# Kernel optimization log

Hardware: AMD Instinct MI355X
Metric: run time of the kernel (lower is better)

## Reference

```python
import jax, jax.numpy as jnp
from jax import lax
import numpy as np


def setup_inputs() -> dict:
    key = jax.random.key(0)
    k1, k2, k3, k4 = jax.random.split(key, 4)
    x = jax.random.normal(k1, (16, 128, 128, 128), dtype=jnp.float32)
    weight = jax.random.normal(k2, (128, 128, 3, 3), dtype=jnp.float32)      # ITPLConv.weight (d, c, kh, kw)
    depth_w = jax.random.normal(k3, (128,), dtype=jnp.float32)               # depthwise 1x1 conv weight (c,1,1,1) flattened
    point_w = jax.random.normal(k4, (128, 128), dtype=jnp.float32)           # pointwise 1x1 conv weight (out, in)
    return {"x": x, "weight": weight, "depth_w": depth_w, "point_w": point_w}


def reference(x, weight, depth_w, point_w):
    # ZeroPad2d(padding=1) on H and W
    xp = jnp.pad(x, ((0, 0), (0, 0), (1, 1), (1, 1)))
    # substract2: unfold(x) - x[:,:,:uh,:uw] broadcast, contracted with weight.
    # Algebraically: conv2d(xp, W, stride=1, VALID) - einsum(xp_crop, W.sum(kh,kw))
    conv = lax.conv_general_dilated(
        xp, weight, window_strides=(1, 1), padding="VALID",
        dimension_numbers=("NCHW", "OIHW", "NCHW"))
    uh, uw = conv.shape[2], conv.shape[3]
    wsum = jnp.sum(weight, axis=(2, 3))                      # (d, c)
    corr = jnp.einsum("nchw,dc->ndhw", xp[:, :, :uh, :uw], wsum)
    sub = conv - corr                                        # (n, d, uh, uw)
    # DWconv: depthwise 1x1 (per-channel scale) then pointwise 1x1
    y = sub * depth_w[None, :, None, None]
    out = jnp.einsum("nchw,oc->nohw", y, point_w)
    return out
```

## Files before the change

kernel.cpp:

```cpp
#include <hip/hip_runtime.h>
#include <hip/hip_bf16.h>


typedef __attribute__((ext_vector_type(8))) short bf16x8;
typedef __attribute__((ext_vector_type(4))) float f32x4;

__device__ inline unsigned short f2bf(float f) {
    unsigned u = __builtin_bit_cast(unsigned, f);
    return (unsigned short)((u + 0x7FFFu + ((u >> 16) & 1u)) >> 16);
}

__device__ inline void gll16(const void* g, void* l) {
    __builtin_amdgcn_global_load_lds((const __attribute__((address_space(1))) void*)g,
                                     (__attribute__((address_space(3))) void*)l, 16, 0, 0);
}

__global__ void fuse_weights_bf16(const float* __restrict__ W,
                                  const float* __restrict__ dw,
                                  const float* __restrict__ P,
                                  unsigned short* __restrict__ w2b) {
    const int c = blockIdx.x;
    const int o = threadIdx.x;
    float acc[9];
#pragma unroll
    for (int t = 0; t < 9; ++t) acc[t] = 0.f;
    for (int d = 0; d < 128; ++d) {
        const float s = P[o * 128 + d] * dw[d];
        const float* wp = W + (size_t)(d * 128 + c) * 9;
        float tsum = 0.f;
#pragma unroll
        for (int t = 0; t < 9; ++t) {
            const float wv = wp[t];
            acc[t] = fmaf(s, wv, acc[t]);
            tsum += wv;
        }
        acc[0] = fmaf(-s, tsum, acc[0]);
    }
#pragma unroll
    for (int t = 0; t < 9; ++t)
        w2b[(t * 128 + o) * 128 + c] = f2bf(acc[t]);
}

__global__ __launch_bounds__(256) void to_nhwc_bf16(const float* __restrict__ x,
                                                    unsigned short* __restrict__ xb,
                                                    unsigned short* __restrict__ zrow) {
    __shared__ __attribute__((aligned(16))) unsigned short ys[128 * 130];
    const int h = blockIdx.x, n = blockIdx.y, tid = (int)threadIdx.x;

    for (int u = tid; u < 4096; u += 256) {
        const int c = u >> 5, w4 = (u & 31) * 4;
        float4 v = *reinterpret_cast<const float4*>(
            x + ((((size_t)n * 128 + c) * 128 + h) * 128 + w4));
        unsigned p0 = (unsigned)f2bf(v.x) | ((unsigned)f2bf(v.y) << 16);
        unsigned p1 = (unsigned)f2bf(v.z) | ((unsigned)f2bf(v.w) << 16);
        *reinterpret_cast<unsigned*>(&ys[c * 130 + w4]) = p0;
        *reinterpret_cast<unsigned*>(&ys[c * 130 + w4 + 2]) = p1;
    }
    __syncthreads();
    for (int u = tid; u < 2048; u += 256) {
        const int w = u >> 4, c8 = u & 15;
        bf16x8 st;
#pragma unroll
        for (int j = 0; j < 8; ++j) st[j] = (short)ys[(c8 * 8 + j) * 130 + w];
        *reinterpret_cast<bf16x8*>(
            xb + ((((size_t)n * 128 + h) * 128 + w) * 128 + c8 * 8)) = st;
    }
    if (h == 0 && n == 0) {
        bf16x8 z = 0;
        for (int u = tid; u < 2048; u += 256)
            *reinterpret_cast<bf16x8*>(zrow + u * 8) = z;
    }
}

#define LDS_CHUNK (3 * 132 * 32)

__global__ __launch_bounds__(256) void itpl_mfma_kernel(
    const unsigned short* __restrict__ xb,
    const unsigned short* __restrict__ w2b,
    const unsigned short* __restrict__ zrow,
    float* __restrict__ out) {
    __shared__ __attribute__((aligned(16))) unsigned short lds[2][LDS_CHUNK];

    const int bid = (int)blockIdx.x;
    const int lin = (bid & 7) * 256 + (bid >> 3);
    const int h = lin & 127, n = lin >> 7;

    const int tid = (int)threadIdx.x;
    const int l = tid & 63, wid = tid >> 6;
    const int wr = wid >> 1, wc = wid & 1;

    f32x4 acc[4][4];
#pragma unroll
    for (int i = 0; i < 4; ++i)
#pragma unroll
        for (int j = 0; j < 4; ++j) acc[i][j] = {0.f, 0.f, 0.f, 0.f};

    if (tid < 48) {
        const int slot = tid & 3, row = tid >> 2;
        const int buf = row / 6, rr = row % 6, r = rr >> 1, wi = (rr & 1) ? 129 : 0;
        bf16x8 z = 0;
        *reinterpret_cast<bf16x8*>(&lds[buf][(r * 132 + wi) * 32 + slot * 8]) = z;
    }

    const size_t nbase = (size_t)n * 128;

    auto stage = [&](int buf, int c0) {
        for (int s = wid * 6; s < wid * 6 + 6; ++s) {
            const int r = s >> 3, seg = s & 7;
            const int hr = h + r - 1;
            const int wl = seg * 16 + (l >> 2);
            const int wi = 1 + wl;
            const int q = (l & 3) ^ ((wi >> 1) & 3);
            const unsigned short* src;
            if ((unsigned)hr < 128u)
                src = xb + (((nbase + hr) * 128 + wl) * 128) + c0 + q * 8;
            else
                src = zrow + (wl * 128 + c0 + q * 8);
            gll16(src, (void*)&lds[buf][(r * 132 + 1 + seg * 16) * 32]);
        }
    };

    auto compute = [&](int buf, int c0) {
        const unsigned short* lb = &lds[buf][0];
#pragma unroll
        for (int t = 0; t < 9; ++t) {
            const int r = t / 3, kw = t % 3;
            bf16x8 bfr[4], afr[4];
#pragma unroll
            for (int ni = 0; ni < 4; ++ni) {
                const int o = wc * 64 + ni * 16 + (l & 15);
                bfr[ni] = *reinterpret_cast<const bf16x8*>(
                    w2b + ((t * 128 + o) * 128 + c0 + (l >> 4) * 8));
            }
#pragma unroll
            for (int mi = 0; mi < 4; ++mi) {
                const int wi = 1 + wr * 64 + mi * 16 + (l & 15) + kw - 1;
                const int slot = (l >> 4) ^ ((wi >> 1) & 3);
                afr[mi] = *reinterpret_cast<const bf16x8*>(
                    lb + (r * 132 + wi) * 32 + slot * 8);
            }
#pragma unroll
            for (int mi = 0; mi < 4; ++mi)
#pragma unroll
                for (int ni = 0; ni < 4; ++ni)
                    acc[mi][ni] = __builtin_amdgcn_mfma_f32_16x16x32_bf16(
                        afr[mi], bfr[ni], acc[mi][ni], 0, 0, 0);
        }
    };

    stage(0, 0);
    __syncthreads();
#pragma unroll
    for (int k = 0; k < 4; ++k) {
        if (k < 3) stage((k + 1) & 1, (k + 1) * 32);
        compute(k & 1, k * 32);
        __syncthreads();
    }

    const size_t ob = (nbase * 128 + h) * 128;
#pragma unroll
    for (int mi = 0; mi < 4; ++mi) {
        const int w = wr * 64 + mi * 16 + (l >> 4) * 4;
#pragma unroll
        for (int ni = 0; ni < 4; ++ni) {
            const int o = wc * 64 + ni * 16 + (l & 15);
            *reinterpret_cast<f32x4*>(out + ob + (size_t)o * 128 * 128 + w) = acc[mi][ni];
        }
    }
}

#define CB 32
__global__ void fuse_weights_kernel(const float* __restrict__ W,
                                    const float* __restrict__ dw,
                                    const float* __restrict__ P,
                                    float* __restrict__ W2) {
    const int c = blockIdx.x;
    const int o = threadIdx.x;
    float acc[9];
#pragma unroll
    for (int t = 0; t < 9; ++t) acc[t] = 0.f;
    for (int d = 0; d < 128; ++d) {
        const float s = P[o * 128 + d] * dw[d];
        const float* wp = W + (size_t)(d * 128 + c) * 9;
        float tsum = 0.f;
#pragma unroll
        for (int t = 0; t < 9; ++t) {
            const float wv = wp[t];
            acc[t] = fmaf(s, wv, acc[t]);
            tsum += wv;
        }
        acc[0] = fmaf(-s, tsum, acc[0]);
    }
#pragma unroll
    for (int t = 0; t < 9; ++t) W2[(c * 9 + t) * 128 + o] = acc[t];
}

__global__ __launch_bounds__(256) void itpl_conv_kernel(const float* __restrict__ x,
                                                        const float* __restrict__ W2,
                                                        float* __restrict__ out) {
    __shared__ float xs[CB][3][132];
    const int h = blockIdx.x;
    const int n = blockIdx.y;
    const int tid = (int)threadIdx.x;
    const int pg = tid & 15;
    const int og = tid >> 4;
    float acc[8][8];
#pragma unroll
    for (int i = 0; i < 8; ++i)
#pragma unroll
        for (int p = 0; p < 8; ++p) acc[i][p] = 0.f;
    for (int c0 = 0; c0 < 128; c0 += CB) {
        __syncthreads();
        for (int g = tid; g < CB * 3 * 32; g += 256) {
            const int f4 = g & 31;
            const int row = g >> 5;
            const int r = row % 3;
            const int c = row / 3;
            const int hr = h + r - 1;
            float4 v = make_float4(0.f, 0.f, 0.f, 0.f);
            if ((unsigned)hr < 128u)
                v = *reinterpret_cast<const float4*>(
                    x + ((((size_t)n * 128 + c0 + c) * 128 + hr) * 128 + f4 * 4));
            float* dst = &xs[c][r][1 + f4 * 4];
            dst[0] = v.x; dst[1] = v.y; dst[2] = v.z; dst[3] = v.w;
        }
        if (tid < CB * 3) {
            const int r = tid % 3;
            const int c = tid / 3;
            xs[c][r][0] = 0.f;
            xs[c][r][129] = 0.f;
        }
        __syncthreads();
        for (int c = 0; c < CB; ++c) {
#pragma unroll
            for (int kh = 0; kh < 3; ++kh) {
                float xr[12];
                const float* xsp = &xs[c][kh][pg * 8];
                *reinterpret_cast<float4*>(&xr[0]) = *reinterpret_cast<const float4*>(xsp);
                *reinterpret_cast<float4*>(&xr[4]) = *reinterpret_cast<const float4*>(xsp + 4);
                *reinterpret_cast<float4*>(&xr[8]) = *reinterpret_cast<const float4*>(xsp + 8);
#pragma unroll
                for (int kw = 0; kw < 3; ++kw) {
                    const float* wp = W2 + (size_t)((c0 + c) * 9 + kh * 3 + kw) * 128 + og * 8;
                    float wv[8];
                    *reinterpret_cast<float4*>(&wv[0]) = *reinterpret_cast<const float4*>(wp);
                    *reinterpret_cast<float4*>(&wv[4]) = *reinterpret_cast<const float4*>(wp + 4);
#pragma unroll
                    for (int i = 0; i < 8; ++i)
#pragma unroll
                        for (int p = 0; p < 8; ++p)
                            acc[i][p] = fmaf(wv[i], xr[p + kw], acc[i][p]);
                }
            }
        }
    }
#pragma unroll
    for (int i = 0; i < 8; ++i) {
        float* op = out + ((((size_t)n * 128 + og * 8 + i) * 128 + h) * 128 + pg * 8);
        *reinterpret_cast<float4*>(op)     = make_float4(acc[i][0], acc[i][1], acc[i][2], acc[i][3]);
        *reinterpret_cast<float4*>(op + 4) = make_float4(acc[i][4], acc[i][5], acc[i][6], acc[i][7]);
    }
}

extern "C" void kernel_launch(void* const* d_in, const int* in_sizes, int n_in,
                              void* d_out, int out_size, void* d_ws, size_t ws_size,
                              hipStream_t stream) {
    const float* x  = (const float*)d_in[0];
    const float* W  = (const float*)d_in[1];
    const float* dw = (const float*)d_in[2];
    const float* P  = (const float*)d_in[3];
    float* out = (float*)d_out;

    const size_t XB_BYTES = 67108864ull;
    const size_t ZR_BYTES = 32768ull;
    const size_t W2B_BYTES = 294912ull;
    if (ws_size >= XB_BYTES + ZR_BYTES + W2B_BYTES) {
        unsigned short* xbw  = (unsigned short*)d_ws;
        unsigned short* zrow = (unsigned short*)((char*)d_ws + XB_BYTES);
        unsigned short* w2b  = (unsigned short*)((char*)d_ws + XB_BYTES + ZR_BYTES);
        fuse_weights_bf16<<<128, 128, 0, stream>>>(W, dw, P, w2b);
        to_nhwc_bf16<<<dim3(128, 16), 256, 0, stream>>>(x, xbw, zrow);
        itpl_mfma_kernel<<<2048, 256, 0, stream>>>(xbw, w2b, zrow, out);
    } else {
        float* W2 = (float*)d_ws;
        fuse_weights_kernel<<<128, 128, 0, stream>>>(W, dw, P, W2);
        itpl_conv_kernel<<<dim3(128, 16), 256, 0, stream>>>(x, W2, out);
    }
}
```

Baseline: 420.9 us.

## Rework NHWC transpose LDS layout, batch weight loads, add occupancy hint

The NCHW-to-NHWC bf16 conversion now packs channel pairs into 32-bit words. It transposes through a padded LDS tile, so the write-out can use single 16-byte LDS reads instead of eight scalar gathers. The main MFMA kernel gets a launch_bounds occupancy hint of 2 blocks per SM. Its inner loop now fetches weight fragments for all three kw taps of a kernel row up front, to expose more memory-level parallelism. The bigger register footprint from the prefetched weights may conflict with the occupancy hint and cause spills.

```diff
diff --git a/kernel.cpp b/kernel.cpp
--- a/kernel.cpp
+++ b/kernel.cpp
@@ -4,6 +4,7 @@
 
 typedef __attribute__((ext_vector_type(8))) short bf16x8;
 typedef __attribute__((ext_vector_type(4))) float f32x4;
+typedef __attribute__((ext_vector_type(2))) unsigned int u32x2;
 
 __device__ inline unsigned short f2bf(float f) {
     unsigned u = __builtin_bit_cast(unsigned, f);
@@ -44,27 +45,44 @@
 __global__ __launch_bounds__(256) void to_nhwc_bf16(const float* __restrict__ x,
                                                     unsigned short* __restrict__ xb,
                                                     unsigned short* __restrict__ zrow) {
-    __shared__ __attribute__((aligned(16))) unsigned short ys[128 * 130];
+    __shared__ __attribute__((aligned(16))) unsigned ys[128 * 68];
     const int h = blockIdx.x, n = blockIdx.y, tid = (int)threadIdx.x;
-
-    for (int u = tid; u < 4096; u += 256) {
-        const int c = u >> 5, w4 = (u & 31) * 4;
-        float4 v = *reinterpret_cast<const float4*>(
-            x + ((((size_t)n * 128 + c) * 128 + h) * 128 + w4));
-        unsigned p0 = (unsigned)f2bf(v.x) | ((unsigned)f2bf(v.y) << 16);
-        unsigned p1 = (unsigned)f2bf(v.z) | ((unsigned)f2bf(v.w) << 16);
-        *reinterpret_cast<unsigned*>(&ys[c * 130 + w4]) = p0;
-        *reinterpret_cast<unsigned*>(&ys[c * 130 + w4 + 2]) = p1;
+    const int wv = tid >> 6, l = tid & 63;
+
+#pragma unroll
+    for (int i = 0; i < 4; ++i) {
+        const int wh = (i & 1) * 64;
+        const int CB0 = (2 * wv + (i >> 1)) * 16;
+        const int c0 = CB0 + 4 * (l >> 4);
+        const int w0 = wh + 4 * (l & 15);
+
+        float4 v[4];
+#pragma unroll
+        for (int r = 0; r < 4; ++r)
+            v[r] = *reinterpret_cast<const float4*>(
+                x + ((((size_t)n * 128 + c0 + r) * 128 + h) * 128 + w0));
+
+        const float* vf = reinterpret_cast<const float*>(v);
+#pragma unroll
+        for (int j = 0; j < 4; ++j) {
+            unsigned u0 = (unsigned)f2bf(vf[0 * 4 + j]) | ((unsigned)f2bf(vf[1 * 4 + j]) << 16);
+            unsigned u1 = (unsigned)f2bf(vf[2 * 4 + j]) | ((unsigned)f2bf(vf[3 * 4 + j]) << 16);
+            u32x2 st; st[0] = u0; st[1] = u1;
+            *reinterpret_cast<u32x2*>(&ys[(w0 + j) * 68 + (c0 >> 1)]) = st;
+        }
     }
     __syncthreads();
-    for (int u = tid; u < 2048; u += 256) {
-        const int w = u >> 4, c8 = u & 15;
-        bf16x8 st;
-#pragma unroll
-        for (int j = 0; j < 8; ++j) st[j] = (short)ys[(c8 * 8 + j) * 130 + w];
+
+#pragma unroll
+    for (int k = 0; k < 8; ++k) {
+        const int u = tid + 256 * k;
+        const int c8 = u & 15, w = u >> 4;
+        bf16x8 val = *reinterpret_cast<const bf16x8*>(
+            reinterpret_cast<const unsigned short*>(ys) + w * 136 + c8 * 8);
         *reinterpret_cast<bf16x8*>(
-            xb + ((((size_t)n * 128 + h) * 128 + w) * 128 + c8 * 8)) = st;
-    }
+            xb + ((((size_t)n * 128 + h) * 128 + w) * 128 + c8 * 8)) = val;
+    }
+
     if (h == 0 && n == 0) {
         bf16x8 z = 0;
         for (int u = tid; u < 2048; u += 256)
@@ -74,7 +92,7 @@
 
 #define LDS_CHUNK (3 * 132 * 32)
 
-__global__ __launch_bounds__(256) void itpl_mfma_kernel(
+__global__ __launch_bounds__(256, 2) void itpl_mfma_kernel(
     const unsigned short* __restrict__ xb,
     const unsigned short* __restrict__ w2b,
     const unsigned short* __restrict__ zrow,
@@ -123,28 +141,34 @@
     auto compute = [&](int buf, int c0) {
         const unsigned short* lb = &lds[buf][0];
 #pragma unroll
-        for (int t = 0; t < 9; ++t) {
-            const int r = t / 3, kw = t % 3;
-            bf16x8 bfr[4], afr[4];
-#pragma unroll
-            for (int ni = 0; ni < 4; ++ni) {
-                const int o = wc * 64 + ni * 16 + (l & 15);
-                bfr[ni] = *reinterpret_cast<const bf16x8*>(
-                    w2b + ((t * 128 + o) * 128 + c0 + (l >> 4) * 8));
+        for (int r = 0; r < 3; ++r) {
+            bf16x8 bfr[3][4];
+#pragma unroll
+            for (int tt = 0; tt < 3; ++tt)
+#pragma unroll
+                for (int ni = 0; ni < 4; ++ni) {
+                    const int t = r * 3 + tt;
+                    const int o = wc * 64 + ni * 16 + (l & 15);
+                    bfr[tt][ni] = *reinterpret_cast<const bf16x8*>(
+                        w2b + ((t * 128 + o) * 128 + c0 + (l >> 4) * 8));
+                }
+#pragma unroll
+            for (int kw = 0; kw < 3; ++kw) {
+                bf16x8 afr[4];
+#pragma unroll
+                for (int mi = 0; mi < 4; ++mi) {
+                    const int wi = 1 + wr * 64 + mi * 16 + (l & 15) + kw - 1;
+                    const int slot = (l >> 4) ^ ((wi >> 1) & 3);
+                    afr[mi] = *reinterpret_cast<const bf16x8*>(
+                        lb + (r * 132 + wi) * 32 + slot * 8);
+                }
+#pragma unroll
+                for (int mi = 0; mi < 4; ++mi)
+#pragma unroll
+                    for (int ni = 0; ni < 4; ++ni)
+                        acc[mi][ni] = __builtin_amdgcn_mfma_f32_16x16x32_bf16(
+                            afr[mi], bfr[kw][ni], acc[mi][ni], 0, 0, 0);
             }
-#pragma unroll
-            for (int mi = 0; mi < 4; ++mi) {
-                const int wi = 1 + wr * 64 + mi * 16 + (l & 15) + kw - 1;
-                const int slot = (l >> 4) ^ ((wi >> 1) & 3);
-                afr[mi] = *reinterpret_cast<const bf16x8*>(
-                    lb + (r * 132 + wi) * 32 + slot * 8);
-            }
-#pragma unroll
-            for (int mi = 0; mi < 4; ++mi)
-#pragma unroll
-                for (int ni = 0; ni < 4; ++ni)
-                    acc[mi][ni] = __builtin_amdgcn_mfma_f32_16x16x32_bf16(
-                        afr[mi], bfr[ni], acc[mi][ni], 0, 0, 0);
         }
     };
 
```

New measurement: 413.2 us. No clear change (-1.9%).
